# Kernel optimization log

Measured on AMD Instinct MI355X. Metric: run time of the kernel, lower is better.

## Reference

```python
import jax, jax.numpy as jnp
import numpy as np

B, V = 128, 128256

def setup_inputs() -> dict:
    key = jax.random.key(0)
    k1, k2, k3, k4, k5 = jax.random.split(key, 5)
    logits = jax.random.normal(k1, (B, V), dtype=jnp.float32) * 2.0
    temperatures = jax.random.uniform(k2, (B,), dtype=jnp.float32) * 0.9 + 0.3  # [0.3, 1.2)
    top_ks = jax.random.randint(k3, (B,), 1, 65, dtype=jnp.int32)               # in [1, 64]
    top_ps = jax.random.uniform(k4, (B,), dtype=jnp.float32) * 0.85 + 0.1       # [0.1, 0.95)
    u = jax.random.uniform(k5, (B,), dtype=jnp.float32)                          # multinomial draw
    return {"logits": logits, "temperatures": temperatures, "top_ks": top_ks,
            "top_ps": top_ps, "u": u}

def reference(logits, temperatures, top_ks, top_ps, u):
    # logits /= temperatures ; probs = softmax(logits)
    probs = jax.nn.softmax(logits / temperatures[:, None], axis=-1)  # [B, V]
    # descending sort (argsort then gather so the permutation is explicit)
    idx = jnp.argsort(-probs, axis=-1)                               # [B, V] int
    probs_sort = jnp.take_along_axis(probs, idx, axis=-1)            # [B, V]
    probs_sum = jnp.cumsum(probs_sort, axis=-1)
    # top-p filter: zero where cumulative mass BEFORE this token exceeds top_p
    # top-k filter: zero beyond rank top_k
    ranks = jnp.arange(probs.shape[-1], dtype=jnp.int32)[None, :]
    mask = (probs_sum - probs_sort > top_ps[:, None]) | (ranks >= top_ks[:, None])
    probs_sort = jnp.where(mask, 0.0, probs_sort)
    # torch code divides by row max (multinomial renormalizes anyway)
    probs_sort = probs_sort / jnp.max(probs_sort, axis=-1, keepdims=True)
    # multinomial(num_samples=1) via inverse-CDF with one uniform per row
    cdf = jnp.cumsum(probs_sort, axis=-1)                            # [B, V]
    r = u[:, None] * cdf[:, -1:]
    sampled_rank = jnp.sum((cdf < r).astype(jnp.int32), axis=-1)     # [B]
    sampled_rank = jnp.clip(sampled_rank, 0, probs.shape[-1] - 1)
    batch_next_token_ids = jnp.take_along_axis(idx, sampled_rank[:, None], axis=-1)[:, 0]
    success = jnp.ones((probs.shape[0],), dtype=jnp.bool_)
    return batch_next_token_ids.astype(jnp.int32), success, probs_sort
```

## Files before the change

### kernel.cpp

```cpp
#include <hip/hip_runtime.h>
#include <math.h>

namespace {
constexpr int kB = 128;
constexpr int kV = 128256;
constexpr int kSplits = 16;
constexpr int kSplit = kV / kSplits;
constexpr int kSplit4 = kSplit / 4;
constexpr int kT1 = 256;
constexpr int kE = 8;
constexpr int kCap = 256;
constexpr int kTop = 64;

using f4v = __attribute__((ext_vector_type(4))) float;

__device__ __forceinline__ unsigned fkey(float y) {
  unsigned u = __float_as_uint(y);
  return ((int)u < 0) ? ~u : (u | 0x80000000u);
}
__device__ __forceinline__ float keyinv(unsigned k) {
  unsigned u = (k & 0x80000000u) ? (k & 0x7fffffffu) : ~k;
  return __uint_as_float(u);
}

__global__ __launch_bounds__(kT1) void k_select(
    const float* __restrict__ logits, const float* __restrict__ temps,
    float* __restrict__ out,
    float* __restrict__ wm, float* __restrict__ wS,
    unsigned long long* __restrict__ wpk) {
  const int sp = blockIdx.x, row = blockIdx.y, tid = threadIdx.x;
  const int lane = tid & 63, wid = tid >> 6;
  __shared__ float wred[4];
  __shared__ float ssum[4];
  __shared__ int cnt2[2][4];
  __shared__ unsigned long long cand[kCap];
  __shared__ int scnt;

  if (tid == 0) scnt = 0;
  const float t = temps[row];
  const float invt = 1.0f / t;
  const size_t rowbase = (size_t)row * kV + (size_t)sp * kSplit;
  const float4* in4 = (const float4*)(logits + rowbase);
  f4v* out4 = (f4v*)(out + 2 * kB + rowbase);
  const float nI = -INFINITY;

  float4 r[kE];
  float m = nI;
#pragma unroll
  for (int e = 0; e < kE; ++e) {
    int f = tid + e * kT1;
    float4 l;
    if (f < kSplit4) l = in4[f];
    else l = make_float4(nI, nI, nI, nI);
    r[e] = l;
    m = fmaxf(m, fmaxf(fmaxf(l.x, l.y), fmaxf(l.z, l.w)));
  }
  for (int o = 32; o; o >>= 1) m = fmaxf(m, __shfl_xor(m, o));
  if (lane == 0) wred[wid] = m;
  __syncthreads();
  const float M = fmaxf(fmaxf(wred[0], wred[1]), fmaxf(wred[2], wred[3]));
  const float My = M / t;
  const float negMy = -My;

  {
    const f4v z4 = {0.f, 0.f, 0.f, 0.f};
#pragma unroll
    for (int e = 0; e < kE; ++e) {
      int f = tid + e * kT1;
      if (f < kSplit4) __builtin_nontemporal_store(z4, out4 + f);
    }
  }

  float s = 0.f;
#pragma unroll
  for (int e = 0; e < kE; ++e) {
    s += __expf(fmaf(r[e].x, invt, negMy));
    s += __expf(fmaf(r[e].y, invt, negMy));
    s += __expf(fmaf(r[e].z, invt, negMy));
    s += __expf(fmaf(r[e].w, invt, negMy));
  }
  for (int o = 32; o; o >>= 1) s += __shfl_xor(s, o);
  if (lane == 0) ssum[wid] = s;
  __syncthreads();
  const float Ssp = ssum[0] + ssum[1] + ssum[2] + ssum[3];

  unsigned lo = 0x00800000u;
  unsigned hi = fkey(M) + 1;
  for (int it = 0; it < 32 && hi - lo > 1; ++it) {
    unsigned mid = lo + ((hi - lo) >> 1);
    if (it == 0) {
      unsigned p0 = fkey(M - 3.0f);
      if (p0 > lo && p0 < hi) mid = p0;
    } else if (it == 1) {
      unsigned p1 = fkey(M - 4.5f);
      if (p1 > lo && p1 < hi) mid = p1;
    }
    const float mf = keyinv(mid);
    int cw = 0;
#pragma unroll
    for (int e = 0; e < kE; ++e) {
      cw += (int)__popcll(__ballot(r[e].x >= mf));
      cw += (int)__popcll(__ballot(r[e].y >= mf));
      cw += (int)__popcll(__ballot(r[e].z >= mf));
      cw += (int)__popcll(__ballot(r[e].w >= mf));
    }
    if (lane == 0) cnt2[it & 1][wid] = cw;
    __syncthreads();
    const int c = cnt2[it & 1][0] + cnt2[it & 1][1] +
                  cnt2[it & 1][2] + cnt2[it & 1][3];
    if (c >= kTop) { lo = mid; if (c <= kCap) break; }
    else hi = mid;
  }
  const float Tf = keyinv(lo);

#pragma unroll
  for (int e = 0; e < kE; ++e) {
    int f = tid + e * kT1;
    const float vals[4] = {r[e].x, r[e].y, r[e].z, r[e].w};
#pragma unroll
    for (int j = 0; j < 4; ++j) {
      const float lv = vals[j];
      if (lv >= Tf) {
        int pos = atomicAdd(&scnt, 1);
        if (pos < kCap)
          cand[pos] = ((unsigned long long)fkey(lv) << 32) |
                      (unsigned)~(unsigned)(sp * kSplit + f * 4 + j);
      }
    }
  }
  __syncthreads();
  const int nc = scnt < kCap ? scnt : kCap;
  unsigned long long v = (tid < nc) ? cand[tid] : 0ULL;

  for (int k2 = 2; k2 <= kCap; k2 <<= 1) {
    for (int j = k2 >> 1; j; j >>= 1) {
      unsigned long long o;
      if (j < 64) {
        o = __shfl_xor(v, j);
      } else {
        __syncthreads();
        cand[tid] = v;
        __syncthreads();
        o = cand[tid ^ j];
      }
      const bool keep_max = (((tid & k2) == 0) == ((tid & j) == 0));
      v = keep_max ? (o > v ? o : v) : (o < v ? o : v);
    }
  }

  if (tid < kTop)
    wpk[((size_t)row * kSplits + sp) * kTop + tid] = v;
  if (tid == 0) {
    wm[row * kSplits + sp] = My;
    wS[row * kSplits + sp] = Ssp;
  }
}

__global__ __launch_bounds__(64) void k_sample(
    const float* __restrict__ temps,
    const int* __restrict__ top_ks, const float* __restrict__ top_ps,
    const float* __restrict__ uin,
    const float* __restrict__ wm, const float* __restrict__ wS,
    const unsigned long long* __restrict__ wpk, float* __restrict__ out) {
  const int row = blockIdx.x;
  const int lane = threadIdx.x;

  float M = -INFINITY;
  for (int s2 = 0; s2 < kSplits; ++s2) M = fmaxf(M, wm[row * kSplits + s2]);
  float S = 0.f;
  for (int s2 = 0; s2 < kSplits; ++s2)
    S += expf(wm[row * kSplits + s2] - M) * wS[row * kSplits + s2];

  const unsigned long long* base = wpk + (size_t)row * (kSplits * kTop);
  unsigned long long v = base[lane];
  for (int s2 = 1; s2 < kSplits; ++s2) {
    unsigned long long b = base[s2 * kTop + (kTop - 1 - lane)];
    v = v > b ? v : b;
#pragma unroll
    for (int j = 32; j; j >>= 1) {
      unsigned long long o = __shfl_xor(v, j);
      v = ((lane & j) == 0) ? (v > o ? v : o) : (v < o ? v : o);
    }
  }
  const float tvl = keyinv((unsigned)(v >> 32)) / temps[row];
  const int til = (int)(~(unsigned)(v & 0xffffffffu));

  const float tp = top_ps[row];
  const int kk = top_ks[row];
  const float uu = uin[row];

  float cum = 0.f, q0 = 0.f;
  float qa_keep = 0.f;
  for (int r2 = 0; r2 < kTop; ++r2) {
    const float tvr = __shfl(tvl, r2);
    const float pr = expf(tvr - M) / S;
    cum += pr;
    const float cb = cum - pr;
    const float q = ((cb > tp) || (r2 >= kk)) ? 0.f : pr;
    if (r2 == 0) q0 = q;
    if (lane == r2) qa_keep = q;
  }
  float tot = 0.f;
  float sv_keep = 0.f, cdf_keep = 0.f;
  for (int r2 = 0; r2 < kTop; ++r2) {
    const float qr = __shfl(qa_keep, r2);
    const float sr = qr / q0;
    tot += sr;
    if (lane == r2) { sv_keep = sr; cdf_keep = tot; }
  }
  const float rth = uu * tot;
  int cnt = (int)__popcll(__ballot(cdf_keep < rth));
  if (cnt > kTop - 1) cnt = kTop - 1;
  const int sampled = __shfl(til, cnt);

  if (lane == 0) {
    out[row] = (float)sampled;
    out[kB + row] = 1.0f;
  }
  out[2 * kB + (size_t)row * kV + lane] = sv_keep;
}
}

extern "C" void kernel_launch(void* const* d_in, const int* in_sizes, int n_in,
                              void* d_out, int out_size, void* d_ws, size_t ws_size,
                              hipStream_t stream) {
  const float* logits = (const float*)d_in[0];
  const float* temps  = (const float*)d_in[1];
  const int*   top_ks = (const int*)d_in[2];
  const float* top_ps = (const float*)d_in[3];
  const float* uin    = (const float*)d_in[4];
  float* out = (float*)d_out;

  float* wm = (float*)d_ws;
  float* wS = wm + kB * kSplits;
  unsigned long long* wpk =
      (unsigned long long*)(wS + kB * kSplits + kB * kSplits);

  k_select<<<dim3(kSplits, kB), kT1, 0, stream>>>(logits, temps, out, wm, wS, wpk);
  k_sample<<<kB, 64, 0, stream>>>(temps, top_ks, top_ps, uin, wm, wS, wpk, out);
}
```

Measured before the change: 55.32 us.

## Fuse select and sample kernels via last-block-done atomic counter

Merges the per-split selection kernel and the per-row sampling kernel into one launch. The last block to finish each row, detected with an agent-scope atomic counter, merges the 16 partial top-64 lists using all four waves before one wave does the sampling. The change also replaces __syncthreads with a lighter LDS-only barrier and skips zero-stores to the first 64 outputs, which the sampler overwrites. This removes a kernel launch and the inter-kernel gap, at the cost of an extra memset launch and fence/atomic traffic.

```diff
diff --git a/kernel.cpp b/kernel.cpp
--- a/kernel.cpp
+++ b/kernel.cpp
@@ -23,11 +23,20 @@
   return __uint_as_float(u);
 }
 
-__global__ __launch_bounds__(kT1) void k_select(
+__device__ __forceinline__ void bar_lds() {
+  __builtin_amdgcn_sched_barrier(0);
+  asm volatile("s_waitcnt lgkmcnt(0)" ::: "memory");
+  __builtin_amdgcn_s_barrier();
+  __builtin_amdgcn_sched_barrier(0);
+}
+
+__global__ __launch_bounds__(kT1) void k_fused(
     const float* __restrict__ logits, const float* __restrict__ temps,
+    const int* __restrict__ top_ks, const float* __restrict__ top_ps,
+    const float* __restrict__ uin,
     float* __restrict__ out,
     float* __restrict__ wm, float* __restrict__ wS,
-    unsigned long long* __restrict__ wpk) {
+    unsigned long long* __restrict__ wpk, int* __restrict__ cnt) {
   const int sp = blockIdx.x, row = blockIdx.y, tid = threadIdx.x;
   const int lane = tid & 63, wid = tid >> 6;
   __shared__ float wred[4];
@@ -35,6 +44,7 @@
   __shared__ int cnt2[2][4];
   __shared__ unsigned long long cand[kCap];
   __shared__ int scnt;
+  __shared__ int lastFlag;
 
   if (tid == 0) scnt = 0;
   const float t = temps[row];
@@ -57,7 +67,7 @@
   }
   for (int o = 32; o; o >>= 1) m = fmaxf(m, __shfl_xor(m, o));
   if (lane == 0) wred[wid] = m;
-  __syncthreads();
+  bar_lds();
   const float M = fmaxf(fmaxf(wred[0], wred[1]), fmaxf(wred[2], wred[3]));
   const float My = M / t;
   const float negMy = -My;
@@ -67,7 +77,8 @@
 #pragma unroll
     for (int e = 0; e < kE; ++e) {
       int f = tid + e * kT1;
-      if (f < kSplit4) __builtin_nontemporal_store(z4, out4 + f);
+      if (f < kSplit4 && (sp != 0 || f >= 16))
+        __builtin_nontemporal_store(z4, out4 + f);
     }
   }
 
@@ -81,7 +92,7 @@
   }
   for (int o = 32; o; o >>= 1) s += __shfl_xor(s, o);
   if (lane == 0) ssum[wid] = s;
-  __syncthreads();
+  bar_lds();
   const float Ssp = ssum[0] + ssum[1] + ssum[2] + ssum[3];
 
   unsigned lo = 0x00800000u;
@@ -105,7 +116,7 @@
       cw += (int)__popcll(__ballot(r[e].w >= mf));
     }
     if (lane == 0) cnt2[it & 1][wid] = cw;
-    __syncthreads();
+    bar_lds();
     const int c = cnt2[it & 1][0] + cnt2[it & 1][1] +
                   cnt2[it & 1][2] + cnt2[it & 1][3];
     if (c >= kTop) { lo = mid; if (c <= kCap) break; }
@@ -128,7 +139,7 @@
       }
     }
   }
-  __syncthreads();
+  bar_lds();
   const int nc = scnt < kCap ? scnt : kCap;
   unsigned long long v = (tid < nc) ? cand[tid] : 0ULL;
 
@@ -138,9 +149,9 @@
       if (j < 64) {
         o = __shfl_xor(v, j);
       } else {
-        __syncthreads();
+        bar_lds();
         cand[tid] = v;
-        __syncthreads();
+        bar_lds();
         o = cand[tid ^ j];
       }
       const bool keep_max = (((tid & k2) == 0) == ((tid & j) == 0));
@@ -154,54 +165,69 @@
     wm[row * kSplits + sp] = My;
     wS[row * kSplits + sp] = Ssp;
   }
-}
-
-__global__ __launch_bounds__(64) void k_sample(
-    const float* __restrict__ temps,
-    const int* __restrict__ top_ks, const float* __restrict__ top_ps,
-    const float* __restrict__ uin,
-    const float* __restrict__ wm, const float* __restrict__ wS,
-    const unsigned long long* __restrict__ wpk, float* __restrict__ out) {
-  const int row = blockIdx.x;
-  const int lane = threadIdx.x;
-
-  float M = -INFINITY;
-  for (int s2 = 0; s2 < kSplits; ++s2) M = fmaxf(M, wm[row * kSplits + s2]);
-  float S = 0.f;
+
+  __syncthreads();
+  if (tid == 0) {
+    __threadfence();
+    int old = __hip_atomic_fetch_add(&cnt[row], 1, __ATOMIC_ACQ_REL,
+                                     __HIP_MEMORY_SCOPE_AGENT);
+    lastFlag = (old == kSplits - 1) ? 1 : 0;
+  }
+  __syncthreads();
+  if (!lastFlag) return;
+
+  __threadfence();
+  const unsigned long long* basek = wpk + (size_t)row * (kSplits * kTop);
+  unsigned long long mv = basek[(size_t)(4 * wid) * kTop + lane];
+#pragma unroll
+  for (int s2 = 1; s2 < 4; ++s2) {
+    unsigned long long b = basek[(size_t)(4 * wid + s2) * kTop + (kTop - 1 - lane)];
+    mv = mv > b ? mv : b;
+#pragma unroll
+    for (int j = 32; j; j >>= 1) {
+      unsigned long long o = __shfl_xor(mv, j);
+      mv = ((lane & j) == 0) ? (mv > o ? mv : o) : (mv < o ? mv : o);
+    }
+  }
+  cand[tid] = mv;
+  bar_lds();
+  if (wid != 0) return;
+
+  mv = cand[lane];
+#pragma unroll
+  for (int s2 = 1; s2 < 4; ++s2) {
+    unsigned long long b = cand[s2 * 64 + (63 - lane)];
+    mv = mv > b ? mv : b;
+#pragma unroll
+    for (int j = 32; j; j >>= 1) {
+      unsigned long long o = __shfl_xor(mv, j);
+      mv = ((lane & j) == 0) ? (mv > o ? mv : o) : (mv < o ? mv : o);
+    }
+  }
+  const float tvl = keyinv((unsigned)(mv >> 32)) / t;
+  const int til = (int)(~(unsigned)(mv & 0xffffffffu));
+
+  float MM = -INFINITY;
+  for (int s2 = 0; s2 < kSplits; ++s2) MM = fmaxf(MM, wm[row * kSplits + s2]);
+  float SS = 0.f;
   for (int s2 = 0; s2 < kSplits; ++s2)
-    S += expf(wm[row * kSplits + s2] - M) * wS[row * kSplits + s2];
-
-  const unsigned long long* base = wpk + (size_t)row * (kSplits * kTop);
-  unsigned long long v = base[lane];
-  for (int s2 = 1; s2 < kSplits; ++s2) {
-    unsigned long long b = base[s2 * kTop + (kTop - 1 - lane)];
-    v = v > b ? v : b;
-#pragma unroll
-    for (int j = 32; j; j >>= 1) {
-      unsigned long long o = __shfl_xor(v, j);
-      v = ((lane & j) == 0) ? (v > o ? v : o) : (v < o ? v : o);
-    }
-  }
-  const float tvl = keyinv((unsigned)(v >> 32)) / temps[row];
-  const int til = (int)(~(unsigned)(v & 0xffffffffu));
+    SS += expf(wm[row * kSplits + s2] - MM) * wS[row * kSplits + s2];
 
   const float tp = top_ps[row];
   const int kk = top_ks[row];
   const float uu = uin[row];
 
-  float cum = 0.f, q0 = 0.f;
-  float qa_keep = 0.f;
+  float cum = 0.f, q0 = 0.f, qa_keep = 0.f;
   for (int r2 = 0; r2 < kTop; ++r2) {
     const float tvr = __shfl(tvl, r2);
-    const float pr = expf(tvr - M) / S;
+    const float pr = expf(tvr - MM) / SS;
     cum += pr;
     const float cb = cum - pr;
     const float q = ((cb > tp) || (r2 >= kk)) ? 0.f : pr;
     if (r2 == 0) q0 = q;
     if (lane == r2) qa_keep = q;
   }
-  float tot = 0.f;
-  float sv_keep = 0.f, cdf_keep = 0.f;
+  float tot = 0.f, sv_keep = 0.f, cdf_keep = 0.f;
   for (int r2 = 0; r2 < kTop; ++r2) {
     const float qr = __shfl(qa_keep, r2);
     const float sr = qr / q0;
@@ -209,9 +235,9 @@
     if (lane == r2) { sv_keep = sr; cdf_keep = tot; }
   }
   const float rth = uu * tot;
-  int cnt = (int)__popcll(__ballot(cdf_keep < rth));
-  if (cnt > kTop - 1) cnt = kTop - 1;
-  const int sampled = __shfl(til, cnt);
+  int cnt2b = (int)__popcll(__ballot(cdf_keep < rth));
+  if (cnt2b > kTop - 1) cnt2b = kTop - 1;
+  const int sampled = __shfl(til, cnt2b);
 
   if (lane == 0) {
     out[row] = (float)sampled;
@@ -235,7 +261,9 @@
   float* wS = wm + kB * kSplits;
   unsigned long long* wpk =
       (unsigned long long*)(wS + kB * kSplits + kB * kSplits);
-
-  k_select<<<dim3(kSplits, kB), kT1, 0, stream>>>(logits, temps, out, wm, wS, wpk);
-  k_sample<<<kB, 64, 0, stream>>>(temps, top_ks, top_ps, uin, wm, wS, wpk, out);
-}
+  int* cnt = (int*)(wpk + (size_t)kB * kSplits * kTop);
+
+  hipMemsetAsync(cnt, 0, kB * sizeof(int), stream);
+  k_fused<<<dim3(kSplits, kB), kT1, 0, stream>>>(logits, temps, top_ks, top_ps,
+                                                 uin, out, wm, wS, wpk, cnt);
+}
```

Measured after the change: 208.3 us. 3.77x slower.
